# Performance work log

Hardware: AMD Instinct MI355X
Metric: run time of the kernel (lower is better)

## Reference

```python
import jax, jax.numpy as jnp
import numpy as np

SCALE, Z, X, Y = 4, 9, 9, 9
INV_SQRT_2PI = 1.0 / np.sqrt(2.0 * np.pi)


def setup_inputs() -> dict:
    key = jax.random.key(0)
    k1, = jax.random.split(key, 1)
    inp = jax.random.normal(k1, (1, 1, 128, 512, 512), dtype=jnp.float32)
    return {
        "inp": inp,
        "mu_z": jnp.asarray(0.0, dtype=jnp.float32),
        "sig_z": jnp.asarray(0.1, dtype=jnp.float32),
        "bet_xy": jnp.asarray(2.0, dtype=jnp.float32),
        "bet_z": jnp.asarray(1.5, dtype=jnp.float32),
    }


def _gen_alf(bet_xy, bet_z):
    # squared distances along each axis; torch's loop overwrites the wrap-around
    # write, so the net result for odd sizes is simply (arange - size//2)**2
    zd = ((jnp.arange(Z) - Z // 2) ** 2).astype(jnp.float32)[:, None, None]
    xd = ((jnp.arange(X) - X // 2) ** 2).astype(jnp.float32)[None, :, None]
    yd = ((jnp.arange(Y) - Y // 2) ** 2).astype(jnp.float32)[None, None, :]
    d_2 = zd / bet_z ** 2 + (xd + yd) / bet_xy ** 2  # (Z, X, Y)
    return jnp.exp(-d_2 / 2) * INV_SQRT_2PI


def reference(inp, mu_z, sig_z, bet_xy, bet_z):
    z0 = jnp.exp(mu_z + 0.5 * sig_z ** 2)
    rec = inp * z0  # (N, 1, D, H, W)
    alf = _gen_alf(bet_xy, bet_z)[None, None]  # (1, 1, Z, X, Y)
    pad_z = (Z - SCALE + 1) // 2
    rec = jax.lax.conv_general_dilated(
        rec, alf,
        window_strides=(SCALE, 1, 1),
        padding=[(pad_z, pad_z), (X // 2, X // 2), (Y // 2, Y // 2)],
        dimension_numbers=("NCDHW", "OIDHW", "NCDHW"),
    )  # (N, 1, D//SCALE, H, W)
    rec = (rec - rec.min()) / (rec.max() - rec.min())
    return rec
```

## Files before the change

### kernel.cpp

```cpp
#include <hip/hip_runtime.h>
#include <float.h>

#define D_IN  128
#define D_OUT 32
#define H     512
#define W     512
#define W4    128
#define HB    8
#define ZR    (HB + 8)
#define NTHR  512
#define NTILE (D_OUT * (H / HB))

__device__ __forceinline__ unsigned f2key(float f) {
    unsigned u = __float_as_uint(f);
    return (u & 0x80000000u) ? ~u : (u | 0x80000000u);
}
__device__ __forceinline__ float key2f(unsigned k) {
    unsigned u = (k & 0x80000000u) ? (k ^ 0x80000000u) : ~k;
    return __uint_as_float(u);
}

__global__ __launch_bounds__(NTHR)
void conv3d_fused(const float* __restrict__ inp, float* __restrict__ out,
                  const float* __restrict__ bxy_p, const float* __restrict__ bz_p,
                  unsigned* __restrict__ fin_u) {
    __shared__ float zbuf[ZR * W];
    __shared__ float hbuf[HB * W];
    __shared__ float smin[8], smax[8];

    const int d  = blockIdx.x >> 6;
    const int h0 = (blockIdx.x & 63) * HB;

    const float bz = bz_p[0], bx = bxy_p[0];
    const float iz = 1.0f / (2.0f * bz * bz);
    const float ix = 1.0f / (2.0f * bx * bx);
    float wz[9], wx[9];
#pragma unroll
    for (int k = 0; k < 9; ++k) {
        float dd = (float)(k - 4);
        wz[k] = expf(-dd * dd * iz);
        wx[k] = expf(-dd * dd * ix);
    }

    const float4* in4 = (const float4*)inp;
    float4* z4 = (float4*)zbuf;
    float4* h4 = (float4*)hbuf;

#pragma unroll
    for (int i = 0; i < (ZR * W4) / NTHR; ++i) {
        int t  = threadIdx.x + i * NTHR;
        int r  = t >> 7;
        int c4 = t & (W4 - 1);
        int h  = h0 - 4 + r;
        float4 acc = make_float4(0.f, 0.f, 0.f, 0.f);
        if ((unsigned)h < H) {
            int base = h * W4 + c4;
#pragma unroll
            for (int k = 0; k < 9; ++k) {
                int din = 4 * d - 3 + k;
                if ((unsigned)din < D_IN) {
                    float4 v = in4[din * (H * W4) + base];
                    acc.x += v.x * wz[k]; acc.y += v.y * wz[k];
                    acc.z += v.z * wz[k]; acc.w += v.w * wz[k];
                }
            }
        }
        z4[t] = acc;
    }
    __syncthreads();

#pragma unroll
    for (int i = 0; i < (HB * W4) / NTHR; ++i) {
        int t  = threadIdx.x + i * NTHR;
        int r  = t >> 7;
        int c4 = t & (W4 - 1);
        float4 acc = make_float4(0.f, 0.f, 0.f, 0.f);
#pragma unroll
        for (int k = 0; k < 9; ++k) {
            float4 v = z4[(r + k) * W4 + c4];
            acc.x += v.x * wx[k]; acc.y += v.y * wx[k];
            acc.z += v.z * wx[k]; acc.w += v.w * wx[k];
        }
        h4[t] = acc;
    }
    __syncthreads();

    float lmin = FLT_MAX, lmax = -FLT_MAX;
    float4* out4 = (float4*)out;
#pragma unroll
    for (int i = 0; i < (HB * W4) / NTHR; ++i) {
        int t  = threadIdx.x + i * NTHR;
        int r  = t >> 7;
        int c4 = t & (W4 - 1);
        float4 zv = make_float4(0.f, 0.f, 0.f, 0.f);
        float4 va = (c4 > 0)      ? h4[r * W4 + c4 - 1] : zv;
        float4 vb =                 h4[r * W4 + c4];
        float4 vc = (c4 < W4 - 1) ? h4[r * W4 + c4 + 1] : zv;
        float win[12] = {va.x, va.y, va.z, va.w,
                         vb.x, vb.y, vb.z, vb.w,
                         vc.x, vc.y, vc.z, vc.w};
        float4 o = make_float4(0.f, 0.f, 0.f, 0.f);
#pragma unroll
        for (int k = 0; k < 9; ++k) {
            o.x += win[k]     * wx[k];
            o.y += win[k + 1] * wx[k];
            o.z += win[k + 2] * wx[k];
            o.w += win[k + 3] * wx[k];
        }
        out4[(d * H + h0 + r) * W4 + c4] = o;
        lmin = fminf(lmin, fminf(fminf(o.x, o.y), fminf(o.z, o.w)));
        lmax = fmaxf(lmax, fmaxf(fmaxf(o.x, o.y), fmaxf(o.z, o.w)));
    }

#pragma unroll
    for (int off = 32; off > 0; off >>= 1) {
        lmin = fminf(lmin, __shfl_down(lmin, off, 64));
        lmax = fmaxf(lmax, __shfl_down(lmax, off, 64));
    }
    int lane = threadIdx.x & 63, wv = threadIdx.x >> 6;
    if (lane == 0) { smin[wv] = lmin; smax[wv] = lmax; }
    __syncthreads();
    if (threadIdx.x == 0) {
        float mn = smin[0], mx = smax[0];
#pragma unroll
        for (int i = 1; i < 8; ++i) { mn = fminf(mn, smin[i]); mx = fmaxf(mx, smax[i]); }
        atomicMin(&fin_u[0], f2key(mn));
        atomicMax(&fin_u[1], f2key(mx));
    }
}

__global__ void norm_kernel(const float* __restrict__ in, float* __restrict__ out,
                            const unsigned* __restrict__ fin_u) {
    int tid = blockIdx.x * blockDim.x + threadIdx.x;
    float mn  = key2f(fin_u[0]);
    float inv = 1.0f / (key2f(fin_u[1]) - mn);
    float4 v = ((const float4*)in)[tid];
    ((float4*)out)[tid] = make_float4((v.x - mn) * inv, (v.y - mn) * inv,
                                      (v.z - mn) * inv, (v.w - mn) * inv);
}

extern "C" void kernel_launch(void* const* d_in, const int* in_sizes, int n_in,
                              void* d_out, int out_size, void* d_ws, size_t ws_size,
                              hipStream_t stream) {
    const float* inp    = (const float*)d_in[0];
    const float* bet_xy = (const float*)d_in[3];
    const float* bet_z  = (const float*)d_in[4];
    float* out = (float*)d_out;

    char* ws = (char*)d_ws;
    unsigned* fin_u = (unsigned*)ws;
    float* bufB = (float*)(ws + 65536);

    hipMemsetAsync(&fin_u[0], 0xFF, 4, stream);
    hipMemsetAsync(&fin_u[1], 0x00, 4, stream);

    conv3d_fused<<<NTILE, NTHR, 0, stream>>>(inp, bufB, bet_xy, bet_z, fin_u);

    const int NTASK = D_OUT * H * W4;
    norm_kernel<<<NTASK / 256, 256, 0, stream>>>(bufB, out, fin_u);
}
```

Baseline: 262.7 us.

## Split fused conv into register-ring Z/H kernel plus separate W-conv kernel

Replaces the single shared-memory tiled kernel with two kernels. The first does the Z and H passes per column, keeping a 9-entry register ring over H so each thread walks a 16-row segment, which removes shared memory and barriers and cuts the H halo overhead from 16/8 to 24/16 rows. The second does the W pass and the min/max reduction. The cost is an extra 32 MB intermediate written to and read back from global memory, plus one more kernel launch.

```diff
diff --git a/kernel.cpp b/kernel.cpp
--- a/kernel.cpp
+++ b/kernel.cpp
@@ -4,12 +4,11 @@
 #define D_IN  128
 #define D_OUT 32
 #define H     512
-#define W     512
 #define W4    128
-#define HB    8
-#define ZR    (HB + 8)
-#define NTHR  512
-#define NTILE (D_OUT * (H / HB))
+#define SEG   16
+#define NSEG  (H / SEG)
+#define ZSTEPS (SEG + 8)
+#define SLICE (H * W4)
 
 __device__ __forceinline__ unsigned f2key(float f) {
     unsigned u = __float_as_uint(f);
@@ -20,110 +19,112 @@
     return __uint_as_float(u);
 }
 
-__global__ __launch_bounds__(NTHR)
-void conv3d_fused(const float* __restrict__ inp, float* __restrict__ out,
-                  const float* __restrict__ bxy_p, const float* __restrict__ bz_p,
-                  unsigned* __restrict__ fin_u) {
-    __shared__ float zbuf[ZR * W];
-    __shared__ float hbuf[HB * W];
-    __shared__ float smin[8], smax[8];
-
-    const int d  = blockIdx.x >> 6;
-    const int h0 = (blockIdx.x & 63) * HB;
+__global__ __launch_bounds__(256)
+void zhconv_kernel(const float* __restrict__ inp, float* __restrict__ out,
+                   const float* __restrict__ bxy_p, const float* __restrict__ bz_p) {
+    const int t   = blockIdx.x * 256 + threadIdx.x;
+    const int c4  = t & (W4 - 1);
+    const int ds  = t >> 7;
+    const int seg = ds & (NSEG - 1);
+    const int d   = ds >> 5;
+    const int hs  = seg * SEG;
 
     const float bz = bz_p[0], bx = bxy_p[0];
     const float iz = 1.0f / (2.0f * bz * bz);
     const float ix = 1.0f / (2.0f * bx * bx);
-    float wz[9], wx[9];
+    float wx[9], wzk[9];
+    const float4* sp[9];
+    const float4* in4 = (const float4*)inp;
 #pragma unroll
     for (int k = 0; k < 9; ++k) {
         float dd = (float)(k - 4);
-        wz[k] = expf(-dd * dd * iz);
+        wx[k] = expf(-dd * dd * ix);
+        int din = 4 * d - 3 + k;
+        bool ok = (din >= 0) && (din < D_IN);
+        int dc = ok ? din : 0;
+        wzk[k] = ok ? expf(-dd * dd * iz) : 0.0f;
+        sp[k]  = in4 + dc * SLICE + c4;
+    }
+
+    float4* out4 = (float4*)out;
+    float4 ring[9];
+#pragma unroll
+    for (int s = 0; s < ZSTEPS; ++s) {
+        const int zrow = hs - 4 + s;
+        float4 zc = make_float4(0.f, 0.f, 0.f, 0.f);
+        if ((unsigned)zrow < H) {
+            const int ro = zrow * W4;
+#pragma unroll
+            for (int k = 0; k < 9; ++k) {
+                float4 v = sp[k][ro];
+                zc.x += v.x * wzk[k]; zc.y += v.y * wzk[k];
+                zc.z += v.z * wzk[k]; zc.w += v.w * wzk[k];
+            }
+        }
+        ring[s % 9] = zc;
+        if (s >= 8) {
+            const int hout = hs + s - 8;
+            float4 acc = make_float4(0.f, 0.f, 0.f, 0.f);
+#pragma unroll
+            for (int k = 0; k < 9; ++k) {
+                float4 v = ring[(s - 8 + k) % 9];
+                acc.x += v.x * wx[k]; acc.y += v.y * wx[k];
+                acc.z += v.z * wx[k]; acc.w += v.w * wx[k];
+            }
+            out4[(d * H + hout) * W4 + c4] = acc;
+        }
+    }
+}
+
+__global__ __launch_bounds__(256)
+void wconv_kernel(const float* __restrict__ in, float* __restrict__ out,
+                  const float* __restrict__ bxy_p, unsigned* __restrict__ fin_u) {
+    const int t   = blockIdx.x * 256 + threadIdx.x;
+    const int c4  = t & (W4 - 1);
+    const int row = t >> 7;
+
+    float bx = bxy_p[0];
+    float ix = 1.0f / (2.0f * bx * bx);
+    float wx[9];
+#pragma unroll
+    for (int k = 0; k < 9; ++k) {
+        float dd = (float)(k - 4);
         wx[k] = expf(-dd * dd * ix);
     }
 
-    const float4* in4 = (const float4*)inp;
-    float4* z4 = (float4*)zbuf;
-    float4* h4 = (float4*)hbuf;
+    const float4* in4 = (const float4*)in;
+    const int base = row * W4;
+    float4 zv = make_float4(0.f, 0.f, 0.f, 0.f);
+    float4 va = (c4 > 0)      ? in4[base + c4 - 1] : zv;
+    float4 vb =                 in4[base + c4];
+    float4 vc = (c4 < W4 - 1) ? in4[base + c4 + 1] : zv;
+    float win[12] = {va.x, va.y, va.z, va.w,
+                     vb.x, vb.y, vb.z, vb.w,
+                     vc.x, vc.y, vc.z, vc.w};
+    float4 o = make_float4(0.f, 0.f, 0.f, 0.f);
+#pragma unroll
+    for (int k = 0; k < 9; ++k) {
+        o.x += win[k]     * wx[k];
+        o.y += win[k + 1] * wx[k];
+        o.z += win[k + 2] * wx[k];
+        o.w += win[k + 3] * wx[k];
+    }
+    ((float4*)out)[base + c4] = o;
 
-#pragma unroll
-    for (int i = 0; i < (ZR * W4) / NTHR; ++i) {
-        int t  = threadIdx.x + i * NTHR;
-        int r  = t >> 7;
-        int c4 = t & (W4 - 1);
-        int h  = h0 - 4 + r;
-        float4 acc = make_float4(0.f, 0.f, 0.f, 0.f);
-        if ((unsigned)h < H) {
-            int base = h * W4 + c4;
-#pragma unroll
-            for (int k = 0; k < 9; ++k) {
-                int din = 4 * d - 3 + k;
-                if ((unsigned)din < D_IN) {
-                    float4 v = in4[din * (H * W4) + base];
-                    acc.x += v.x * wz[k]; acc.y += v.y * wz[k];
-                    acc.z += v.z * wz[k]; acc.w += v.w * wz[k];
-                }
-            }
-        }
-        z4[t] = acc;
-    }
-    __syncthreads();
-
-#pragma unroll
-    for (int i = 0; i < (HB * W4) / NTHR; ++i) {
-        int t  = threadIdx.x + i * NTHR;
-        int r  = t >> 7;
-        int c4 = t & (W4 - 1);
-        float4 acc = make_float4(0.f, 0.f, 0.f, 0.f);
-#pragma unroll
-        for (int k = 0; k < 9; ++k) {
-            float4 v = z4[(r + k) * W4 + c4];
-            acc.x += v.x * wx[k]; acc.y += v.y * wx[k];
-            acc.z += v.z * wx[k]; acc.w += v.w * wx[k];
-        }
-        h4[t] = acc;
-    }
-    __syncthreads();
-
-    float lmin = FLT_MAX, lmax = -FLT_MAX;
-    float4* out4 = (float4*)out;
-#pragma unroll
-    for (int i = 0; i < (HB * W4) / NTHR; ++i) {
-        int t  = threadIdx.x + i * NTHR;
-        int r  = t >> 7;
-        int c4 = t & (W4 - 1);
-        float4 zv = make_float4(0.f, 0.f, 0.f, 0.f);
-        float4 va = (c4 > 0)      ? h4[r * W4 + c4 - 1] : zv;
-        float4 vb =                 h4[r * W4 + c4];
-        float4 vc = (c4 < W4 - 1) ? h4[r * W4 + c4 + 1] : zv;
-        float win[12] = {va.x, va.y, va.z, va.w,
-                         vb.x, vb.y, vb.z, vb.w,
-                         vc.x, vc.y, vc.z, vc.w};
-        float4 o = make_float4(0.f, 0.f, 0.f, 0.f);
-#pragma unroll
-        for (int k = 0; k < 9; ++k) {
-            o.x += win[k]     * wx[k];
-            o.y += win[k + 1] * wx[k];
-            o.z += win[k + 2] * wx[k];
-            o.w += win[k + 3] * wx[k];
-        }
-        out4[(d * H + h0 + r) * W4 + c4] = o;
-        lmin = fminf(lmin, fminf(fminf(o.x, o.y), fminf(o.z, o.w)));
-        lmax = fmaxf(lmax, fmaxf(fmaxf(o.x, o.y), fmaxf(o.z, o.w)));
-    }
-
+    float lmin = fminf(fminf(o.x, o.y), fminf(o.z, o.w));
+    float lmax = fmaxf(fmaxf(o.x, o.y), fmaxf(o.z, o.w));
 #pragma unroll
     for (int off = 32; off > 0; off >>= 1) {
         lmin = fminf(lmin, __shfl_down(lmin, off, 64));
         lmax = fmaxf(lmax, __shfl_down(lmax, off, 64));
     }
+    __shared__ float smin[4], smax[4];
     int lane = threadIdx.x & 63, wv = threadIdx.x >> 6;
     if (lane == 0) { smin[wv] = lmin; smax[wv] = lmax; }
     __syncthreads();
     if (threadIdx.x == 0) {
-        float mn = smin[0], mx = smax[0];
-#pragma unroll
-        for (int i = 1; i < 8; ++i) { mn = fminf(mn, smin[i]); mx = fmaxf(mx, smax[i]); }
+        float mn = fminf(fminf(smin[0], smin[1]), fminf(smin[2], smin[3]));
+        float mx = fmaxf(fmaxf(smax[0], smax[1]), fmaxf(smax[2], smax[3]));
         atomicMin(&fin_u[0], f2key(mn));
         atomicMax(&fin_u[1], f2key(mx));
     }
@@ -149,13 +150,17 @@
 
     char* ws = (char*)d_ws;
     unsigned* fin_u = (unsigned*)ws;
-    float* bufB = (float*)(ws + 65536);
+    float* bufA = (float*)(ws + 65536);
+    float* bufB = (float*)(ws + 65536 + (size_t)33554432);
 
     hipMemsetAsync(&fin_u[0], 0xFF, 4, stream);
     hipMemsetAsync(&fin_u[1], 0x00, 4, stream);
 
-    conv3d_fused<<<NTILE, NTHR, 0, stream>>>(inp, bufB, bet_xy, bet_z, fin_u);
+    const int K1_THREADS = D_OUT * NSEG * W4;
+    zhconv_kernel<<<K1_THREADS / 256, 256, 0, stream>>>(inp, bufA, bet_xy, bet_z);
 
     const int NTASK = D_OUT * H * W4;
+    wconv_kernel<<<NTASK / 256, 256, 0, stream>>>(bufA, bufB, bet_xy, fin_u);
+
     norm_kernel<<<NTASK / 256, 256, 0, stream>>>(bufB, out, fin_u);
 }
```

Measured after the change: 416.5 us. +58.5%, slower.
